# Kernel tuning notes

Hardware: AMD Instinct MI355X
Metric: run time of the kernel (lower is better)

## Reference

```python
import jax, jax.numpy as jnp
import numpy as np

DIM = 64
HEADS = 8
P = 4  # polarizations
EPS = 1e-12


def _conv2d(x, w, b, groups):
    # x: [N,C,H,W], w: [O, C//groups, kh, kw] (torch OIHW), stride 1, SAME padding
    y = jax.lax.conv_general_dilated(
        x, w, window_strides=(1, 1), padding='SAME',
        dimension_numbers=('NCHW', 'OIHW', 'NCHW'), feature_group_count=groups)
    return y + b[None, :, None, None]


def setup_inputs() -> dict:
    key = jax.random.key(0)
    ks = jax.random.split(key, 12)
    B, C, H, W = 4, DIM, 128, 128
    s = 1.0 / np.sqrt(C)
    x_in = jax.random.normal(ks[0], (B * P, C, H, W), dtype=jnp.float32)
    mask = jax.random.uniform(ks[1], (B * P, C, H, W), dtype=jnp.float32)
    wq = jax.random.normal(ks[2], (C, C), dtype=jnp.float32) * s
    wk = jax.random.normal(ks[3], (C, C), dtype=jnp.float32) * s
    wv = jax.random.normal(ks[4], (C, C), dtype=jnp.float32) * s
    w_proj = jax.random.normal(ks[5], (C, C), dtype=jnp.float32) * s
    b_proj = jax.random.normal(ks[6], (C,), dtype=jnp.float32) * 0.01
    rescale = jnp.ones((HEADS, 1, 1), dtype=jnp.float32)
    dw_w = jax.random.normal(ks[7], (C, 1, 3, 3), dtype=jnp.float32) * (1.0 / 3.0)
    dw_b = jax.random.normal(ks[8], (C,), dtype=jnp.float32) * 0.01
    pw_w = jax.random.normal(ks[9], (C, C, 1, 1), dtype=jnp.float32) * s
    pw_b = jax.random.normal(ks[10], (C,), dtype=jnp.float32) * 0.01
    return {'x_in': x_in, 'mask': mask, 'wq': wq, 'wk': wk, 'wv': wv,
            'w_proj': w_proj, 'b_proj': b_proj, 'rescale': rescale,
            'dw_w': dw_w, 'dw_b': dw_b, 'pw_w': pw_w, 'pw_b': pw_b}


def reference(x_in, mask, wq, wk, wv, w_proj, b_proj, rescale, dw_w, dw_b, pw_w, pw_b):
    bp, c, h, w = x_in.shape
    b_num = bp // P
    dh = c // HEADS
    # 'b p c h w -> (b h w) p c'
    x = x_in.reshape(b_num, P, c, h, w).transpose(0, 3, 4, 1, 2).reshape(b_num * h * w, P, c)
    # torch Linear (no bias): x @ W.T
    q = jnp.einsum('bpc,dc->bpd', x, wq)
    k = jnp.einsum('bpc,dc->bpd', x, wk)
    v = jnp.einsum('bpc,dc->bpd', x, wv)
    # 'b p (h c) -> b h p c'
    q = q.reshape(-1, P, HEADS, dh).transpose(0, 2, 1, 3)
    k = k.reshape(-1, P, HEADS, dh).transpose(0, 2, 1, 3)
    v = v.reshape(-1, P, HEADS, dh).transpose(0, 2, 1, 3)
    # L2 normalize along head dim (torch F.normalize: clamp_min(eps))
    q = q / jnp.maximum(jnp.linalg.norm(q, axis=-1, keepdims=True), EPS)
    k = k / jnp.maximum(jnp.linalg.norm(k, axis=-1, keepdims=True), EPS)
    atten = jnp.einsum('bhpc,bhqc->bhpq', q, k) * rescale  # rescale: [heads,1,1]
    # mask branch: depthwise 3x3 -> GELU(exact) -> pointwise 1x1
    mg = _conv2d(mask, dw_w, dw_b, groups=c)
    mg = jax.nn.gelu(mg, approximate=False)
    mg = _conv2d(mg, pw_w, pw_b, groups=1)
    mg = mg.reshape(b_num, P, c, h, w).mean(axis=2)  # [b,p,h,w]
    mb = mg.transpose(0, 2, 3, 1).reshape(b_num * h * w, P)  # '(b h w) p'
    mask_bias = mb[:, None, :] - mb[:, :, None]  # [B, p, p]
    atten = atten + mask_bias[:, None, :, :]
    atten = jax.nn.softmax(atten, axis=-1)
    out = jnp.einsum('bhpq,bhqc->bhpc', atten, v)
    out = out.transpose(0, 2, 1, 3).reshape(-1, P, c)  # 'b h p c -> b p (h c)'
    out = jnp.einsum('bpc,dc->bpd', out, w_proj) + b_proj
    # '(b h w) p c -> b p c h w' -> [(b p), c, h, w]
    out = out.reshape(b_num, h, w, P, c).transpose(0, 3, 4, 1, 2)
    return out.reshape(b_num * P, c, h, w)
```

## Files before the change

### kernel.cpp

```cpp
#include <hip/hip_runtime.h>
#include <hip/hip_bf16.h>

#define HSZ 128
#define WSZ 128
#define HWSZ (HSZ*WSZ)
#define NB 4

#define OFF_MB 0

typedef unsigned short u16;
typedef __attribute__((ext_vector_type(8))) short bf16x8;
typedef __attribute__((ext_vector_type(4))) float f32x4;

__device__ __forceinline__ float bf2f(u16 u) {
    return __uint_as_float(((unsigned int)u) << 16);
}
__device__ __forceinline__ unsigned int cvt_pk_bf16(float lo, float hi) {
    __hip_bfloat162 h = __float22bfloat162_rn(make_float2(lo, hi));
    return *(unsigned int*)&h;
}
__device__ __forceinline__ int sswz(int s) { return s ^ (s >> 3); }
__device__ __forceinline__ float qp1(float x) {
    return __uint_as_float(__builtin_amdgcn_mov_dpp(__float_as_uint(x), 0xB1, 0xF, 0xF, false));
}
__device__ __forceinline__ float qp2(float x) {
    return __uint_as_float(__builtin_amdgcn_mov_dpp(__float_as_uint(x), 0x4E, 0xF, 0xF, false));
}
__device__ __forceinline__ float qp3(float x) {
    return __uint_as_float(__builtin_amdgcn_mov_dpp(__float_as_uint(x), 0x1B, 0xF, 0xF, false));
}
__device__ __forceinline__ bf16x8 load_bfrag(const float* W, int drow, int k0) {
    float4 a = *(const float4*)(W + drow*64 + k0);
    float4 b = *(const float4*)(W + drow*64 + k0 + 4);
    unsigned int u[4];
    u[0] = cvt_pk_bf16(a.x, a.y); u[1] = cvt_pk_bf16(a.z, a.w);
    u[2] = cvt_pk_bf16(b.x, b.y); u[3] = cvt_pk_bf16(b.z, b.w);
    return *(bf16x8*)u;
}

__global__ __launch_bounds__(1024) void mask_kernel(const float* __restrict__ mask,
                                                    const float* __restrict__ dww,
                                                    const float* __restrict__ dwb,
                                                    const float* __restrict__ pww,
                                                    float* __restrict__ ws) {
    __shared__ float red[4][256][4];
    __shared__ float cmS[64];
    int tid = threadIdx.x;
    if (tid < 64) {
        float s = 0.f;
        for (int co = 0; co < 64; ++co) s += pww[co*64 + tid];
        cmS[tid] = s * (1.0f/64.0f);
    }
    __syncthreads();
    int bid = blockIdx.x;
    int bp = bid >> 4;
    int hg = bid & 15;
    int cq = tid >> 8;
    int t = tid & 255;
    int h = hg*8 + (t >> 5);
    int w0 = (t & 31) << 2;
    const float* mb_ = mask + (size_t)bp*64*HWSZ;
    int hm = h > 0 ? h-1 : 0;
    int hp = h < 127 ? h+1 : 127;
    float vt = h > 0 ? 1.f : 0.f;
    float vb = h < 127 ? 1.f : 0.f;
    float vl = w0 > 0 ? 1.f : 0.f;
    float vr = w0 < 124 ? 1.f : 0.f;
    int wl = w0 > 0 ? w0-1 : 0;
    int wr = w0 < 124 ? w0+4 : 127;
    float acc0=0.f, acc1=0.f, acc2=0.f, acc3=0.f;
    for (int ci = 0; ci < 16; ++ci) {
        int c = cq*16 + ci;
        const float* rc = mb_ + c*HWSZ;
        const float* r0 = rc + hm*WSZ;
        const float* r1 = rc + h*WSZ;
        const float* r2 = rc + hp*WSZ;
        float4 m0 = *(const float4*)(r0 + w0);
        float4 m1 = *(const float4*)(r1 + w0);
        float4 m2 = *(const float4*)(r2 + w0);
        float L0 = r0[wl]*vl, L1 = r1[wl]*vl, L2 = r2[wl]*vl;
        float R0 = r0[wr]*vr, R1 = r1[wr]*vr, R2 = r2[wr]*vr;
        float w00 = dww[c*9+0]*vt, w01 = dww[c*9+1]*vt, w02 = dww[c*9+2]*vt;
        float w10 = dww[c*9+3],    w11 = dww[c*9+4],    w12 = dww[c*9+5];
        float w20 = dww[c*9+6]*vb, w21 = dww[c*9+7]*vb, w22 = dww[c*9+8]*vb;
        float bb = dwb[c];
        float s0 = bb + w00*L0   + w01*m0.x + w02*m0.y
                      + w10*L1   + w11*m1.x + w12*m1.y
                      + w20*L2   + w21*m2.x + w22*m2.y;
        float s1 = bb + w00*m0.x + w01*m0.y + w02*m0.z
                      + w10*m1.x + w11*m1.y + w12*m1.z
                      + w20*m2.x + w21*m2.y + w22*m2.z;
        float s2 = bb + w00*m0.y + w01*m0.z + w02*m0.w
                      + w10*m1.y + w11*m1.z + w12*m1.w
                      + w20*m2.y + w21*m2.z + w22*m2.w;
        float s3 = bb + w00*m0.z + w01*m0.w + w02*R0
                      + w10*m1.z + w11*m1.w + w12*R1
                      + w20*m2.z + w21*m2.w + w22*R2;
        float cmc = cmS[c];
        acc0 += cmc * (0.5f*s0*(1.f + erff(s0*0.70710678118654752f)));
        acc1 += cmc * (0.5f*s1*(1.f + erff(s1*0.70710678118654752f)));
        acc2 += cmc * (0.5f*s2*(1.f + erff(s2*0.70710678118654752f)));
        acc3 += cmc * (0.5f*s3*(1.f + erff(s3*0.70710678118654752f)));
    }
    red[cq][t][0] = acc0;
    red[cq][t][1] = acc1;
    red[cq][t][2] = acc2;
    red[cq][t][3] = acc3;
    __syncthreads();
    if (tid < 256) {
        int b = bp >> 2, p = bp & 3;
        size_t base = (size_t)b*HWSZ + h*WSZ + w0;
        #pragma unroll
        for (int e = 0; e < 4; ++e) {
            float v = red[0][tid][e] + red[1][tid][e] + red[2][tid][e] + red[3][tid][e];
            ws[OFF_MB + (base+e)*4 + p] = v;
        }
    }
}

__global__ __launch_bounds__(512, 6) void attn_kernel(const float* __restrict__ x_in,
                                                      const float* __restrict__ wq,
                                                      const float* __restrict__ wk,
                                                      const float* __restrict__ wv,
                                                      const float* __restrict__ wp,
                                                      const float* __restrict__ bpj,
                                                      const float* __restrict__ rsc,
                                                      const float* __restrict__ ws,
                                                      float* __restrict__ out) {
    __shared__ u16 smem[24576];
    u16* ldsAV = smem;
    u16* ldsQ  = smem + 8192;
    u16* ldsK  = smem + 16384;
    unsigned int* ldsAV32 = (unsigned int*)ldsAV;
    unsigned int* ldsQ32  = (unsigned int*)ldsQ;

    int t = threadIdx.x;
    int lane = t & 63;
    int wid = __builtin_amdgcn_readfirstlane(t >> 6);
    int dq = wid & 3;
    int half = wid >> 2;
    int n15 = lane & 15;
    int quad = lane >> 4;
    int b = blockIdx.x >> 9;
    int hw0 = (blockIdx.x & 511) << 5;

    bf16x8 fq0 = load_bfrag(wq, dq*16 + n15, quad*8);
    bf16x8 fq1 = load_bfrag(wq, dq*16 + n15, 32 + quad*8);
    bf16x8 fk0 = load_bfrag(wk, dq*16 + n15, quad*8);
    bf16x8 fk1 = load_bfrag(wk, dq*16 + n15, 32 + quad*8);
    bf16x8 fv0 = load_bfrag(wv, dq*16 + n15, quad*8);
    bf16x8 fv1 = load_bfrag(wv, dq*16 + n15, 32 + quad*8);
    bf16x8 fp0 = load_bfrag(wp, dq*16 + n15, quad*8);
    bf16x8 fp1 = load_bfrag(wp, dq*16 + n15, 32 + quad*8);
    float4 b4 = *(const float4*)(bpj + dq*16 + quad*4);

    for (int it = 0; it < 2; ++it) {
        int i = t + (it << 9);
        int rp = i >> 3, l4 = i & 7;
        int p = rp >> 5, cp = rp & 31;
        int c0 = cp*2;
        const float* r0 = x_in + (size_t)(b*256 + p*64 + c0)*HWSZ + hw0 + l4*4;
        float4 v0 = *(const float4*)r0;
        float4 v1 = *(const float4*)(r0 + HWSZ);
        int kt = c0 >> 5, qd = (c0 >> 3) & 3, j2 = (c0 & 7) >> 1;
        float a0v[4] = {v0.x, v0.y, v0.z, v0.w};
        float a1v[4] = {v1.x, v1.y, v1.z, v1.w};
        #pragma unroll
        for (int e = 0; e < 4; ++e) {
            int tau = (p << 5) + (l4 << 2) + e;
            int slot = (tau & 15) | (qd << 4);
            ldsAV32[((tau >> 4)*2 + kt)*256 + sswz(slot)*4 + j2] = cvt_pk_bf16(a0v[e], a1v[e]);
        }
    }
    __syncthreads();

    int sl8 = sswz(lane)*8;
    uint2 vreg[4];
    #pragma unroll
    for (int m = 0; m < 4; ++m) {
        int mt = half*4 + m;
        bf16x8 a0 = *(const bf16x8*)(ldsAV + mt*1024 + sl8);
        bf16x8 a1 = *(const bf16x8*)(ldsAV + mt*1024 + 512 + sl8);
        f32x4 aq = {0.f,0.f,0.f,0.f};
        f32x4 ak = {0.f,0.f,0.f,0.f};
        f32x4 av = {0.f,0.f,0.f,0.f};
        aq = __builtin_amdgcn_mfma_f32_16x16x32_bf16(fq0, a0, aq, 0, 0, 0);
        aq = __builtin_amdgcn_mfma_f32_16x16x32_bf16(fq1, a1, aq, 0, 0, 0);
        ak = __builtin_amdgcn_mfma_f32_16x16x32_bf16(fk0, a0, ak, 0, 0, 0);
        ak = __builtin_amdgcn_mfma_f32_16x16x32_bf16(fk1, a1, ak, 0, 0, 0);
        av = __builtin_amdgcn_mfma_f32_16x16x32_bf16(fv0, a0, av, 0, 0, 0);
        av = __builtin_amdgcn_mfma_f32_16x16x32_bf16(fv1, a1, av, 0, 0, 0);
        int tg = mt*16 + n15;
        int tok = (tg & 31)*4 + (tg >> 5);
        int base = dq*4 + quad;
        int X = n15 & 7;
        int g = (base & 1) | ((((base >> 1) ^ X) & 7) << 1);
        int off = tok*64 + g*4;
        uint2 pq, pk;
        pq.x = cvt_pk_bf16(aq[0], aq[1]); pq.y = cvt_pk_bf16(aq[2], aq[3]);
        pk.x = cvt_pk_bf16(ak[0], ak[1]); pk.y = cvt_pk_bf16(ak[2], ak[3]);
        *(uint2*)(ldsQ + off) = pq;
        *(uint2*)(ldsK + off) = pk;
        vreg[m].x = cvt_pk_bf16(av[0], av[1]);
        vreg[m].y = cvt_pk_bf16(av[2], av[3]);
    }
    __syncthreads();
    #pragma unroll
    for (int m = 0; m < 4; ++m) {
        int tg = (half*4 + m)*16 + n15;
        int tok = (tg & 31)*4 + (tg >> 5);
        int base = dq*4 + quad;
        int X = n15 & 7;
        int g = (base & 1) | ((((base >> 1) ^ X) & 7) << 1);
        *(uint2*)(ldsAV + tok*64 + g*4) = vreg[m];
    }
    __syncthreads();

    uint4 yreg[2];
    int p2 = t & 3;
    int hd = (t >> 2) & 7;
    int pix0 = t >> 5;
    float rs = rsc[hd];
    #pragma unroll
    for (int u = 0; u < 2; ++u) {
        int pix = pix0 + u*16;
        int tok = pix*4 + p2;
        int off = tok*64 + ((hd ^ (pix & 7)) << 3);
        bf16x8 q8 = *(const bf16x8*)(ldsQ + off);
        bf16x8 k8 = *(const bf16x8*)(ldsK + off);
        bf16x8 v8 = *(const bf16x8*)(ldsAV + off);
        float qv[8], kv[8];
        float sq = 0.f, sk = 0.f;
        #pragma unroll
        for (int j = 0; j < 8; ++j) {
            qv[j] = bf2f((u16)q8[j]);
            kv[j] = bf2f((u16)k8[j]);
            sq += qv[j]*qv[j];
            sk += kv[j]*kv[j];
        }
        float iq = rsqrtf(fmaxf(sq, 1e-24f));
        float ik = rsqrtf(fmaxf(sk, 1e-24f));
        float d0 = 0.f, d1 = 0.f, d2 = 0.f, d3 = 0.f;
        #pragma unroll
        for (int j = 0; j < 8; ++j) {
            float kj = kv[j];
            d0 += qv[j]*kj;
            d1 += qv[j]*qp1(kj);
            d2 += qv[j]*qp2(kj);
            d3 += qv[j]*qp3(kj);
        }
        float mbp = ws[OFF_MB + ((size_t)b*HWSZ + hw0 + pix)*4 + p2];
        float iqrs = iq * rs;
        float s0 = d0*(iqrs*ik)      + mbp;
        float s1 = d1*(iqrs*qp1(ik)) + qp1(mbp);
        float s2 = d2*(iqrs*qp2(ik)) + qp2(mbp);
        float s3 = d3*(iqrs*qp3(ik)) + qp3(mbp);
        float mx = fmaxf(fmaxf(s0, s1), fmaxf(s2, s3));
        float e0 = __expf(s0-mx), e1 = __expf(s1-mx);
        float e2 = __expf(s2-mx), e3 = __expf(s3-mx);
        float inv = 1.0f / (e0+e1+e2+e3);
        float w0 = e0*inv, w1 = e1*inv, w2 = e2*inv, w3 = e3*inv;
        float y[8];
        #pragma unroll
        for (int j = 0; j < 8; ++j) {
            float vj = bf2f((u16)v8[j]);
            y[j] = w0*vj + w1*qp1(vj) + w2*qp2(vj) + w3*qp3(vj);
        }
        yreg[u].x = cvt_pk_bf16(y[0], y[1]);
        yreg[u].y = cvt_pk_bf16(y[2], y[3]);
        yreg[u].z = cvt_pk_bf16(y[4], y[5]);
        yreg[u].w = cvt_pk_bf16(y[6], y[7]);
    }
    __syncthreads();
    #pragma unroll
    for (int u = 0; u < 2; ++u) {
        int pix = pix0 + u*16;
        int tau = (p2 << 5) + pix;
        int slot = (tau & 15) | ((hd & 3) << 4);
        *(uint4*)(ldsQ32 + ((tau >> 4)*2 + (hd >> 2))*256 + sswz(slot)*4) = yreg[u];
    }
    __syncthreads();

    #pragma unroll
    for (int m = 0; m < 4; ++m) {
        int mt = half*4 + m;
        bf16x8 a0 = *(const bf16x8*)(ldsQ + mt*1024 + sl8);
        bf16x8 a1 = *(const bf16x8*)(ldsQ + mt*1024 + 512 + sl8);
        f32x4 ao = {0.f,0.f,0.f,0.f};
        ao = __builtin_amdgcn_mfma_f32_16x16x32_bf16(fp0, a0, ao, 0, 0, 0);
        ao = __builtin_amdgcn_mfma_f32_16x16x32_bf16(fp1, a1, ao, 0, 0, 0);
        int p = mt >> 1;
        int px = (mt & 1)*16 + n15;
        size_t obase = ((size_t)((b*4 + p)*64 + dq*16 + quad*4))*HWSZ + hw0 + px;
        out[obase]          = ao[0] + b4.x;
        out[obase +   HWSZ] = ao[1] + b4.y;
        out[obase + 2*HWSZ] = ao[2] + b4.z;
        out[obase + 3*HWSZ] = ao[3] + b4.w;
    }
}

extern "C" void kernel_launch(void* const* d_in, const int* in_sizes, int n_in,
                              void* d_out, int out_size, void* d_ws, size_t ws_size,
                              hipStream_t stream) {
    const float* x_in  = (const float*)d_in[0];
    const float* mask  = (const float*)d_in[1];
    const float* wq    = (const float*)d_in[2];
    const float* wk    = (const float*)d_in[3];
    const float* wv    = (const float*)d_in[4];
    const float* wproj = (const float*)d_in[5];
    const float* bproj = (const float*)d_in[6];
    const float* resc  = (const float*)d_in[7];
    const float* dww   = (const float*)d_in[8];
    const float* dwb   = (const float*)d_in[9];
    const float* pww   = (const float*)d_in[10];
    float* ws = (float*)d_ws;
    float* outp = (float*)d_out;

    hipLaunchKernelGGL(mask_kernel, dim3(256), dim3(1024), 0, stream,
                       mask, dww, dwb, pww, ws);
    hipLaunchKernelGGL(attn_kernel, dim3(2048), dim3(512), 0, stream,
                       x_in, wq, wk, wv, wproj, bproj, resc, ws, outp);
}
```

Before: 240.9 us.

## Fuse mask depthwise-GELU-pointwise branch into attention kernel via shared-memory bias

Removes the separate mask kernel and computes the per-pixel mask bias inside each attention block. Each block reads the 3x3 neighbourhood of the mask for its 32 pixels and 4 polarizations and reduces the bias with LDS atomics. This drops a kernel launch and the workspace round-trip. The weight-fragment loads are also moved closer to where they are used, which is meant to lower register pressure. In exchange, each block recomputes the column sums of pww and re-reads halo rows of the mask, since neighbouring row blocks overlap. It also adds shared-memory atomics and an extra barrier.

Result: slower. 248.5 us (+3.1%).

```diff
diff --git a/kernel.cpp b/kernel.cpp
--- a/kernel.cpp
+++ b/kernel.cpp
@@ -5,8 +5,6 @@
 #define WSZ 128
 #define HWSZ (HSZ*WSZ)
 #define NB 4
-
-#define OFF_MB 0
 
 typedef unsigned short u16;
 typedef __attribute__((ext_vector_type(8))) short bf16x8;
@@ -38,99 +36,25 @@
     return *(bf16x8*)u;
 }
 
-__global__ __launch_bounds__(1024) void mask_kernel(const float* __restrict__ mask,
-                                                    const float* __restrict__ dww,
-                                                    const float* __restrict__ dwb,
-                                                    const float* __restrict__ pww,
-                                                    float* __restrict__ ws) {
-    __shared__ float red[4][256][4];
-    __shared__ float cmS[64];
-    int tid = threadIdx.x;
-    if (tid < 64) {
-        float s = 0.f;
-        for (int co = 0; co < 64; ++co) s += pww[co*64 + tid];
-        cmS[tid] = s * (1.0f/64.0f);
-    }
-    __syncthreads();
-    int bid = blockIdx.x;
-    int bp = bid >> 4;
-    int hg = bid & 15;
-    int cq = tid >> 8;
-    int t = tid & 255;
-    int h = hg*8 + (t >> 5);
-    int w0 = (t & 31) << 2;
-    const float* mb_ = mask + (size_t)bp*64*HWSZ;
-    int hm = h > 0 ? h-1 : 0;
-    int hp = h < 127 ? h+1 : 127;
-    float vt = h > 0 ? 1.f : 0.f;
-    float vb = h < 127 ? 1.f : 0.f;
-    float vl = w0 > 0 ? 1.f : 0.f;
-    float vr = w0 < 124 ? 1.f : 0.f;
-    int wl = w0 > 0 ? w0-1 : 0;
-    int wr = w0 < 124 ? w0+4 : 127;
-    float acc0=0.f, acc1=0.f, acc2=0.f, acc3=0.f;
-    for (int ci = 0; ci < 16; ++ci) {
-        int c = cq*16 + ci;
-        const float* rc = mb_ + c*HWSZ;
-        const float* r0 = rc + hm*WSZ;
-        const float* r1 = rc + h*WSZ;
-        const float* r2 = rc + hp*WSZ;
-        float4 m0 = *(const float4*)(r0 + w0);
-        float4 m1 = *(const float4*)(r1 + w0);
-        float4 m2 = *(const float4*)(r2 + w0);
-        float L0 = r0[wl]*vl, L1 = r1[wl]*vl, L2 = r2[wl]*vl;
-        float R0 = r0[wr]*vr, R1 = r1[wr]*vr, R2 = r2[wr]*vr;
-        float w00 = dww[c*9+0]*vt, w01 = dww[c*9+1]*vt, w02 = dww[c*9+2]*vt;
-        float w10 = dww[c*9+3],    w11 = dww[c*9+4],    w12 = dww[c*9+5];
-        float w20 = dww[c*9+6]*vb, w21 = dww[c*9+7]*vb, w22 = dww[c*9+8]*vb;
-        float bb = dwb[c];
-        float s0 = bb + w00*L0   + w01*m0.x + w02*m0.y
-                      + w10*L1   + w11*m1.x + w12*m1.y
-                      + w20*L2   + w21*m2.x + w22*m2.y;
-        float s1 = bb + w00*m0.x + w01*m0.y + w02*m0.z
-                      + w10*m1.x + w11*m1.y + w12*m1.z
-                      + w20*m2.x + w21*m2.y + w22*m2.z;
-        float s2 = bb + w00*m0.y + w01*m0.z + w02*m0.w
-                      + w10*m1.y + w11*m1.z + w12*m1.w
-                      + w20*m2.y + w21*m2.z + w22*m2.w;
-        float s3 = bb + w00*m0.z + w01*m0.w + w02*R0
-                      + w10*m1.z + w11*m1.w + w12*R1
-                      + w20*m2.z + w21*m2.w + w22*R2;
-        float cmc = cmS[c];
-        acc0 += cmc * (0.5f*s0*(1.f + erff(s0*0.70710678118654752f)));
-        acc1 += cmc * (0.5f*s1*(1.f + erff(s1*0.70710678118654752f)));
-        acc2 += cmc * (0.5f*s2*(1.f + erff(s2*0.70710678118654752f)));
-        acc3 += cmc * (0.5f*s3*(1.f + erff(s3*0.70710678118654752f)));
-    }
-    red[cq][t][0] = acc0;
-    red[cq][t][1] = acc1;
-    red[cq][t][2] = acc2;
-    red[cq][t][3] = acc3;
-    __syncthreads();
-    if (tid < 256) {
-        int b = bp >> 2, p = bp & 3;
-        size_t base = (size_t)b*HWSZ + h*WSZ + w0;
-        #pragma unroll
-        for (int e = 0; e < 4; ++e) {
-            float v = red[0][tid][e] + red[1][tid][e] + red[2][tid][e] + red[3][tid][e];
-            ws[OFF_MB + (base+e)*4 + p] = v;
-        }
-    }
-}
-
 __global__ __launch_bounds__(512, 6) void attn_kernel(const float* __restrict__ x_in,
+                                                      const float* __restrict__ mask,
                                                       const float* __restrict__ wq,
                                                       const float* __restrict__ wk,
                                                       const float* __restrict__ wv,
                                                       const float* __restrict__ wp,
                                                       const float* __restrict__ bpj,
                                                       const float* __restrict__ rsc,
-                                                      const float* __restrict__ ws,
+                                                      const float* __restrict__ dww,
+                                                      const float* __restrict__ dwb,
+                                                      const float* __restrict__ pww,
                                                       float* __restrict__ out) {
     __shared__ u16 smem[24576];
     u16* ldsAV = smem;
     u16* ldsQ  = smem + 8192;
     u16* ldsK  = smem + 16384;
+    __shared__ float ldsW[640];
+    __shared__ float cmS[64];
+    __shared__ float mbS[128];
     unsigned int* ldsAV32 = (unsigned int*)ldsAV;
     unsigned int* ldsQ32  = (unsigned int*)ldsQ;
 
@@ -144,15 +68,73 @@
     int b = blockIdx.x >> 9;
     int hw0 = (blockIdx.x & 511) << 5;
 
-    bf16x8 fq0 = load_bfrag(wq, dq*16 + n15, quad*8);
-    bf16x8 fq1 = load_bfrag(wq, dq*16 + n15, 32 + quad*8);
-    bf16x8 fk0 = load_bfrag(wk, dq*16 + n15, quad*8);
-    bf16x8 fk1 = load_bfrag(wk, dq*16 + n15, 32 + quad*8);
-    bf16x8 fv0 = load_bfrag(wv, dq*16 + n15, quad*8);
-    bf16x8 fv1 = load_bfrag(wv, dq*16 + n15, 32 + quad*8);
-    bf16x8 fp0 = load_bfrag(wp, dq*16 + n15, quad*8);
-    bf16x8 fp1 = load_bfrag(wp, dq*16 + n15, 32 + quad*8);
-    float4 b4 = *(const float4*)(bpj + dq*16 + quad*4);
+    for (int i = t; i < 640; i += 512) ldsW[i] = (i < 576) ? dww[i] : dwb[i - 576];
+    if (t < 128) mbS[t] = 0.f;
+    if (t < 64) {
+        float s = 0.f;
+        #pragma unroll
+        for (int co = 0; co < 64; ++co) s += pww[co*64 + t];
+        cmS[t] = s * (1.0f/64.0f);
+    }
+    __syncthreads();
+
+    {
+        int pxg = t & 7;
+        int cp  = (t >> 3) & 3;
+        int cs  = t >> 5;
+        int h   = hw0 >> 7;
+        int w0c = (hw0 & 127) + pxg*4;
+        int hm = h > 0 ? h-1 : 0;
+        int hp = h < 127 ? h+1 : 127;
+        float vt = h > 0 ? 1.f : 0.f;
+        float vb = h < 127 ? 1.f : 0.f;
+        float vl = w0c > 0 ? 1.f : 0.f;
+        float vr = w0c < 124 ? 1.f : 0.f;
+        int wl = w0c > 0 ? w0c-1 : 0;
+        int wr = w0c < 124 ? w0c+4 : 127;
+        const float* mp_ = mask + (size_t)(b*4 + cp)*64*HWSZ;
+        float a0=0.f, a1=0.f, a2=0.f, a3=0.f;
+        #pragma unroll
+        for (int ci = 0; ci < 4; ++ci) {
+            int c = cs*4 + ci;
+            const float* rc = mp_ + c*HWSZ;
+            const float* r0 = rc + hm*WSZ;
+            const float* r1 = rc + h*WSZ;
+            const float* r2 = rc + hp*WSZ;
+            float4 m0 = *(const float4*)(r0 + w0c);
+            float4 m1 = *(const float4*)(r1 + w0c);
+            float4 m2 = *(const float4*)(r2 + w0c);
+            float L0 = r0[wl]*vl, L1 = r1[wl]*vl, L2 = r2[wl]*vl;
+            float R0 = r0[wr]*vr, R1 = r1[wr]*vr, R2 = r2[wr]*vr;
+            const float* w9 = ldsW + c*9;
+            float w00 = w9[0]*vt, w01 = w9[1]*vt, w02 = w9[2]*vt;
+            float w10 = w9[3],    w11 = w9[4],    w12 = w9[5];
+            float w20 = w9[6]*vb, w21 = w9[7]*vb, w22 = w9[8]*vb;
+            float bb = ldsW[576 + c];
+            float s0 = bb + w00*L0   + w01*m0.x + w02*m0.y
+                          + w10*L1   + w11*m1.x + w12*m1.y
+                          + w20*L2   + w21*m2.x + w22*m2.y;
+            float s1 = bb + w00*m0.x + w01*m0.y + w02*m0.z
+                          + w10*m1.x + w11*m1.y + w12*m1.z
+                          + w20*m2.x + w21*m2.y + w22*m2.z;
+            float s2 = bb + w00*m0.y + w01*m0.z + w02*m0.w
+                          + w10*m1.y + w11*m1.z + w12*m1.w
+                          + w20*m2.y + w21*m2.z + w22*m2.w;
+            float s3 = bb + w00*m0.z + w01*m0.w + w02*R0
+                          + w10*m1.z + w11*m1.w + w12*R1
+                          + w20*m2.z + w21*m2.w + w22*R2;
+            float cmc = cmS[c];
+            a0 += cmc * (0.5f*s0*(1.f + erff(s0*0.70710678118654752f)));
+            a1 += cmc * (0.5f*s1*(1.f + erff(s1*0.70710678118654752f)));
+            a2 += cmc * (0.5f*s2*(1.f + erff(s2*0.70710678118654752f)));
+            a3 += cmc * (0.5f*s3*(1.f + erff(s3*0.70710678118654752f)));
+        }
+        int mb0 = cp*32 + pxg*4;
+        atomicAdd(&mbS[mb0 + 0], a0);
+        atomicAdd(&mbS[mb0 + 1], a1);
+        atomicAdd(&mbS[mb0 + 2], a2);
+        atomicAdd(&mbS[mb0 + 3], a3);
+    }
 
     for (int it = 0; it < 2; ++it) {
         int i = t + (it << 9);
@@ -172,6 +154,13 @@
             ldsAV32[((tau >> 4)*2 + kt)*256 + sswz(slot)*4 + j2] = cvt_pk_bf16(a0v[e], a1v[e]);
         }
     }
+
+    bf16x8 fq0 = load_bfrag(wq, dq*16 + n15, quad*8);
+    bf16x8 fq1 = load_bfrag(wq, dq*16 + n15, 32 + quad*8);
+    bf16x8 fk0 = load_bfrag(wk, dq*16 + n15, quad*8);
+    bf16x8 fk1 = load_bfrag(wk, dq*16 + n15, 32 + quad*8);
+    bf16x8 fv0 = load_bfrag(wv, dq*16 + n15, quad*8);
+    bf16x8 fv1 = load_bfrag(wv, dq*16 + n15, 32 + quad*8);
     __syncthreads();
 
     int sl8 = sswz(lane)*8;
@@ -249,7 +238,7 @@
             d2 += qv[j]*qp2(kj);
             d3 += qv[j]*qp3(kj);
         }
-        float mbp = ws[OFF_MB + ((size_t)b*HWSZ + hw0 + pix)*4 + p2];
+        float mbp = mbS[p2*32 + pix];
         float iqrs = iq * rs;
         float s0 = d0*(iqrs*ik)      + mbp;
         float s1 = d1*(iqrs*qp1(ik)) + qp1(mbp);
@@ -281,6 +270,9 @@
     }
     __syncthreads();
 
+    bf16x8 fp0 = load_bfrag(wp, dq*16 + n15, quad*8);
+    bf16x8 fp1 = load_bfrag(wp, dq*16 + n15, 32 + quad*8);
+    float4 b4 = *(const float4*)(bpj + dq*16 + quad*4);
     #pragma unroll
     for (int m = 0; m < 4; ++m) {
         int mt = half*4 + m;
@@ -313,11 +305,9 @@
     const float* dww   = (const float*)d_in[8];
     const float* dwb   = (const float*)d_in[9];
     const float* pww   = (const float*)d_in[10];
-    float* ws = (float*)d_ws;
     float* outp = (float*)d_out;
 
-    hipLaunchKernelGGL(mask_kernel, dim3(256), dim3(1024), 0, stream,
-                       mask, dww, dwb, pww, ws);
     hipLaunchKernelGGL(attn_kernel, dim3(2048), dim3(512), 0, stream,
-                       x_in, wq, wk, wv, wproj, bproj, resc, ws, outp);
-}
+                       x_in, mask, wq, wk, wv, wproj, bproj, resc,
+                       dww, dwb, pww, outp);
+}
```
